# Kernel tuning notes

Measured on AMD Instinct MI355X. Metric: run time of the kernel, lower is better.

Reference implementation:

```python
import jax, jax.numpy as jnp
import numpy as np

K = 3    # spline degree
NUM = 5  # grid intervals


def _extended_grid(in_dim):
    # pykan default grid_range=[-1,1], extended by K knots of spacing h on each side
    h = 2.0 / NUM
    g = jnp.linspace(-1.0 - K * h, 1.0 + K * h, NUM + 2 * K + 1, dtype=jnp.float32)
    return jnp.tile(g[None, :], (in_dim, 1))  # (in_dim, NUM+2K+1)


def _bspline_basis(x, grid):
    # Cox-de Boor recursion, matches pykan B_batch.
    # x: (..., in_dim); grid: (in_dim, NUM+2K+1) -> (..., in_dim, NUM+K)
    xe = x[..., None]
    B = ((xe >= grid[:, :-1]) & (xe < grid[:, 1:])).astype(x.dtype)
    for d in range(1, K + 1):
        left = (xe - grid[:, :-(d + 1)]) / (grid[:, d:-1] - grid[:, :-(d + 1)])
        right = (grid[:, d + 1:] - xe) / (grid[:, d + 1:] - grid[:, 1:-d])
        B = left * B[..., :-1] + right * B[..., 1:]
    return B


def _kan_layer(x, grid, coef, scale_base, scale_sp):
    # pykan KANLayer.forward (mask == 1): y = sum_i scale_base*silu(x) + scale_sp*spline(x)
    base = jax.nn.silu(x)                              # (..., in)
    Bx = _bspline_basis(x, grid)                       # (..., in, NUM+K)
    spl = jnp.einsum('...ik,iok->...io', Bx, coef)     # (..., in, out)
    y = scale_base * base[..., None] + scale_sp * spl  # (..., in, out)
    return y.sum(axis=-2)                              # (..., out)


def setup_inputs() -> dict:
    key = jax.random.key(0)
    seq_len, in_dim, hidden_dim, out_dim = 8192, 128, 512, 128
    nb = NUM + K
    hu_in = in_dim + hidden_dim
    ks = jax.random.split(key, 5)
    return {
        "x": jax.random.normal(ks[0], (seq_len, in_dim), jnp.float32),
        "h0": jnp.zeros((hidden_dim,), jnp.float32),
        "hu_grid": _extended_grid(hu_in),
        "hu_coef": jax.random.normal(ks[1], (hu_in, hidden_dim, nb), jnp.float32) * 0.1,
        "hu_scale_base": jax.random.normal(ks[2], (hu_in, hidden_dim), jnp.float32) / np.sqrt(hu_in).astype(np.float32),
        "hu_scale_sp": jnp.ones((hu_in, hidden_dim), jnp.float32) / np.float32(np.sqrt(hu_in)),
        "out_grid": _extended_grid(hidden_dim),
        "out_coef": jax.random.normal(ks[3], (hidden_dim, out_dim, nb), jnp.float32) * 0.1,
        "out_scale_base": jax.random.normal(ks[4], (hidden_dim, out_dim), jnp.float32) / np.float32(np.sqrt(hidden_dim)),
        "out_scale_sp": jnp.ones((hidden_dim, out_dim), jnp.float32) / np.float32(np.sqrt(hidden_dim)),
    }


def reference(x, h0, hu_grid, hu_coef, hu_scale_base, hu_scale_sp,
              out_grid, out_coef, out_scale_base, out_scale_sp):
    # Sequential KAN-cell recurrence over time (torch for-loop -> lax.scan)
    def step(h, x_t):
        inp = jnp.concatenate([x_t, h])  # (in_dim + hidden_dim,)
        h_new = _kan_layer(inp, hu_grid, hu_coef, hu_scale_base, hu_scale_sp)
        return h_new, h_new

    _, hidden_states = jax.lax.scan(step, h0, x)  # (seq, hidden)
    outputs = _kan_layer(hidden_states, out_grid, out_coef, out_scale_base, out_scale_sp)
    return outputs, hidden_states
```

## Files before the change

### kernel.cpp

```cpp
#include <hip/hip_runtime.h>
#include <math.h>

#define SEQ 8192
#define IN_DIM 128
#define HID 512
#define OUT_DIM 128
#define NK 9
#define KNOTS 12

#define WS_W9HU  0
#define WS_WSEQP 589824
#define WS_XPART (WS_WSEQP + 1179648)
#define WS_HCOMM (WS_XPART + 4194304)
#define WS_TOTAL (WS_HCOMM + 4194304)

#define SENTINEL 0x7FA0DEADu

#define NWG 32
#define TPB2 512

__device__ __forceinline__ int brow(int ib) { return ib*3 + (ib >> 4); }
__device__ __forceinline__ int boff(int row) { return row*12 + ((row >> 2) << 2); }

__device__ __forceinline__ unsigned bf16rne(float f) {
    unsigned b = __float_as_uint(f);
    return (b + 0x7fffu + ((b >> 16) & 1u)) >> 16;
}
__device__ __forceinline__ float blo(unsigned p) { return __uint_as_float(p << 16); }
__device__ __forceinline__ float bhi(unsigned p) { return __uint_as_float(p & 0xffff0000u); }

__device__ __forceinline__ void load_knots(const float* gptr, float* g, float* invA) {
    #pragma unroll
    for (int j = 0; j < KNOTS; ++j) g[j] = gptr[j];
    #pragma unroll
    for (int d = 1; d <= 3; ++d) {
        #pragma unroll
        for (int j = 0; j < 11; ++j) {
            if (j + d <= 11) invA[(d-1)*11 + j] = 1.0f / (g[j+d] - g[j]);
        }
    }
}

__device__ __forceinline__ void basis9(float x, const float* g, const float* invA, float* out) {
    float B[11];
    #pragma unroll
    for (int j = 0; j < 11; ++j)
        B[j] = (x >= g[j] && x < g[j+1]) ? 1.0f : 0.0f;
    #pragma unroll
    for (int d = 1; d <= 3; ++d) {
        #pragma unroll
        for (int j = 0; j < 11; ++j) {
            if (j + d < 11) {
                float left  = (x - g[j]) * invA[(d-1)*11 + j];
                float right = (g[j+d+1] - x) * invA[(d-1)*11 + j + 1];
                B[j] = left * B[j] + right * B[j+1];
            }
        }
    }
    #pragma unroll
    for (int j = 0; j < 8; ++j) out[j] = B[j];
    out[8] = x / (1.0f + expf(-x));
}

__global__ __launch_bounds__(256) void build1_kernel(
    const float* __restrict__ hu_coef, const float* __restrict__ hu_sb, const float* __restrict__ hu_ssp,
    float* __restrict__ ws)
{
    int idx = blockIdx.x * blockDim.x + threadIdx.x;
    int stride = gridDim.x * blockDim.x;
    const int N1 = 128 * 9 * 512;
    for (int p = idx; p < N1; p += stride) {
        int o = p & 511; int k = (p >> 9) % 9; int i = p / 4608;
        float v = (k < 8) ? hu_ssp[i*HID + o] * hu_coef[(i*HID + o)*8 + k] : hu_sb[i*HID + o];
        ws[WS_W9HU + p] = v;
    }
    unsigned* WP = (unsigned*)(ws + WS_WSEQP);
    const int N2 = 32 * 512 * 72;
    for (int p = idx; p < N2; p += stride) {
        int slot = p % 72; int th = (p / 72) & 511; int blk = p / (72 * 512);
        int q = th >> 2, oq = th & 3;
        unsigned pr;
        if (slot < 64) {
            int r = slot >> 4, j = (slot >> 2) & 3, kp = slot & 3;
            int gi = IN_DIM + 4*q + r;
            int o  = blk*16 + oq*4 + j;
            float wlo = hu_ssp[gi*HID + o] * hu_coef[(gi*HID + o)*8 + 2*kp];
            float whi = hu_ssp[gi*HID + o] * hu_coef[(gi*HID + o)*8 + 2*kp + 1];
            pr = bf16rne(wlo) | (bf16rne(whi) << 16);
        } else {
            int e = slot - 64;
            int r = e >> 1, jp = e & 1;
            int gi = IN_DIM + 4*q + r;
            int o0 = blk*16 + oq*4 + 2*jp;
            int o1 = o0 + 1;
            pr = bf16rne(hu_sb[gi*HID + o0]) | (bf16rne(hu_sb[gi*HID + o1]) << 16);
        }
        WP[p] = pr;
    }
    unsigned* hc = (unsigned*)(ws + WS_HCOMM);
    for (int p = idx; p < SEQ*HID; p += stride) hc[p] = SENTINEL;
}

__global__ __launch_bounds__(256) void build2_kernel(
    const float* __restrict__ out_coef, const float* __restrict__ out_sb, const float* __restrict__ out_ssp,
    float* __restrict__ ws)
{
    int idx = blockIdx.x * blockDim.x + threadIdx.x;
    int stride = gridDim.x * blockDim.x;
    const int N = 512 * 9 * 128;
    for (int p = idx; p < N; p += stride) {
        int o = p & 127; int k = (p >> 7) % 9; int i = p / 1152;
        float v = (k < 8) ? out_ssp[i*OUT_DIM + o] * out_coef[(i*OUT_DIM + o)*8 + k] : out_sb[i*OUT_DIM + o];
        ws[WS_W9HU + p] = v;
    }
}

#define R1 4
__global__ __launch_bounds__(256) void xpart_kernel(
    const float* __restrict__ X, const float* __restrict__ hu_grid, float* __restrict__ ws)
{
    const int tid = threadIdx.x;
    const int t0 = blockIdx.x * R1;
    const float* W9 = ws + WS_W9HU;
    float* xpart = ws + WS_XPART;
    float g[KNOTS], invA[33];
    load_knots(hu_grid, g, invA);

    __shared__ float4 bas4[R1*IN_DIM*3 + (R1*IN_DIM)/16];
    #pragma unroll
    for (int rep = 0; rep < 2; ++rep) {
        int idx = tid + rep*256;
        int r = idx >> 7, i = idx & 127;
        float bv[9];
        basis9(X[(t0 + r)*IN_DIM + i], g, invA, bv);
        int rb = brow(idx);
        bas4[rb]   = make_float4(bv[0], bv[1], bv[2], bv[3]);
        bas4[rb+1] = make_float4(bv[4], bv[5], bv[6], bv[7]);
        bas4[rb+2] = make_float4(bv[8], 0.f, 0.f, 0.f);
    }
    __syncthreads();

    float acc[R1][2];
    #pragma unroll
    for (int r = 0; r < R1; ++r) { acc[r][0] = 0.f; acc[r][1] = 0.f; }

    for (int i = 0; i < IN_DIM; ++i) {
        float w1[9], w2[9];
        #pragma unroll
        for (int k = 0; k < 9; ++k) {
            w1[k] = W9[(i*NK+k)*HID + tid];
            w2[k] = W9[(i*NK+k)*HID + tid + 256];
        }
        #pragma unroll
        for (int r = 0; r < R1; ++r) {
            const float* rp = (const float*)&bas4[brow(r*IN_DIM + i)];
            float4 b0 = ((const float4*)rp)[0], b1 = ((const float4*)rp)[1];
            float b8 = rp[8];
            float s1 = w1[0]*b0.x + w1[1]*b0.y + w1[2]*b0.z + w1[3]*b0.w
                     + w1[4]*b1.x + w1[5]*b1.y + w1[6]*b1.z + w1[7]*b1.w + w1[8]*b8;
            float s2 = w2[0]*b0.x + w2[1]*b0.y + w2[2]*b0.z + w2[3]*b0.w
                     + w2[4]*b1.x + w2[5]*b1.y + w2[6]*b1.z + w2[7]*b1.w + w2[8]*b8;
            acc[r][0] += s1; acc[r][1] += s2;
        }
    }
    #pragma unroll
    for (int r = 0; r < R1; ++r) {
        xpart[(t0+r)*HID + tid]       = acc[r][0];
        xpart[(t0+r)*HID + tid + 256] = acc[r][1];
    }
}

__global__ __launch_bounds__(TPB2, 1) void seq_kernel(
    const float* __restrict__ h0, const float* __restrict__ hu_grid,
    const unsigned* __restrict__ WP,
    const float* __restrict__ xpart,
    unsigned* __restrict__ hcomm,
    float* __restrict__ hs_out)
{
    const int tid  = threadIdx.x;
    const int blk  = blockIdx.x;
    const int lane = tid & 63;
    const int wave = tid >> 6;
    const int oq   = tid & 3;
    const int q    = tid >> 2;
    const float g0 = hu_grid[0];
    const float inv_h = 1.0f / (hu_grid[1] - hu_grid[0]);

    unsigned wsp[4][4][4];
    unsigned wsl[4][2];
    {
        const uint4* Wb = (const uint4*)(WP + ((size_t)blk*512 + tid)*72);
        #pragma unroll
        for (int r = 0; r < 4; ++r) {
            #pragma unroll
            for (int j = 0; j < 4; ++j) {
                uint4 v = Wb[r*4 + j];
                wsp[r][j][0] = v.x; wsp[r][j][1] = v.y; wsp[r][j][2] = v.z; wsp[r][j][3] = v.w;
            }
        }
        uint4 s0 = Wb[16];
        uint4 s1 = Wb[17];
        wsl[0][0]=s0.x; wsl[0][1]=s0.y; wsl[1][0]=s0.z; wsl[1][1]=s0.w;
        wsl[2][0]=s1.x; wsl[2][1]=s1.y; wsl[3][0]=s1.z; wsl[3][1]=s1.w;
    }

    __shared__ float basf[6656];
    __shared__ float red[8][4][4];

    for (int t = 0; t < SEQ; ++t) {
        float xf = (tid < 16) ? xpart[(size_t)t*HID + blk*16 + tid] : 0.0f;

        float hv;
        if (t == 0) {
            hv = h0[tid];
        } else {
            const unsigned* pp = &hcomm[(size_t)(t-1)*HID + tid];
            unsigned u = __hip_atomic_load(pp, __ATOMIC_RELAXED, __HIP_MEMORY_SCOPE_AGENT);
            int sp = 0;
            while (u == SENTINEL && ++sp < (1 << 24))
                u = __hip_atomic_load(pp, __ATOMIC_RELAXED, __HIP_MEMORY_SCOPE_AGENT);
            hv = __uint_as_float(u);
        }

        {
            float* rowp = basf + boff(tid);
            float tq = (hv - g0) * inv_h;
            float cf = floorf(tq);
            float u  = tq - cf;
            int   c  = (int)cf;
            float si = hv * __builtin_amdgcn_rcpf(1.0f + __expf(-hv));
            ((float4*)rowp)[0] = make_float4(0.f, 0.f, 0.f, 0.f);
            ((float4*)rowp)[1] = make_float4(0.f, 0.f, 0.f, 0.f);
            rowp[8] = si;
            if (c >= 0 && c <= 10) {
                float um = 1.0f - u, u2 = u*u, u3 = u2*u;
                float P0 = um*um*um*(1.0f/6.0f);
                float P1 = 0.5f*u3 - u2 + (2.0f/3.0f);
                float P2 = -0.5f*u3 + 0.5f*u2 + 0.5f*u + (1.0f/6.0f);
                float P3 = u3*(1.0f/6.0f);
                int j0 = c - 3;
                if (j0     >= 0)              rowp[j0]     = P0;
                if (j0 + 1 >= 0 && j0+1 <= 7) rowp[j0 + 1] = P1;
                if (j0 + 2 >= 0 && j0+2 <= 7) rowp[j0 + 2] = P2;
                if (j0 + 3 <= 7)              rowp[j0 + 3] = P3;
            }
        }
        __syncthreads();

        float p0 = 0.f, p1 = 0.f, p2 = 0.f, p3 = 0.f;
        #pragma unroll
        for (int r = 0; r < 4; ++r) {
            const float* rp = basf + boff(4*q + r);
            float4 b0 = ((const float4*)rp)[0], b1 = ((const float4*)rp)[1];
            float b8 = rp[8];
            p0 += blo(wsp[r][0][0])*b0.x + bhi(wsp[r][0][0])*b0.y + blo(wsp[r][0][1])*b0.z + bhi(wsp[r][0][1])*b0.w
                + blo(wsp[r][0][2])*b1.x + bhi(wsp[r][0][2])*b1.y + blo(wsp[r][0][3])*b1.z + bhi(wsp[r][0][3])*b1.w
                + blo(wsl[r][0])*b8;
            p1 += blo(wsp[r][1][0])*b0.x + bhi(wsp[r][1][0])*b0.y + blo(wsp[r][1][1])*b0.z + bhi(wsp[r][1][1])*b0.w
                + blo(wsp[r][1][2])*b1.x + bhi(wsp[r][1][2])*b1.y + blo(wsp[r][1][3])*b1.z + bhi(wsp[r][1][3])*b1.w
                + bhi(wsl[r][0])*b8;
            p2 += blo(wsp[r][2][0])*b0.x + bhi(wsp[r][2][0])*b0.y + blo(wsp[r][2][1])*b0.z + bhi(wsp[r][2][1])*b0.w
                + blo(wsp[r][2][2])*b1.x + bhi(wsp[r][2][2])*b1.y + blo(wsp[r][2][3])*b1.z + bhi(wsp[r][2][3])*b1.w
                + blo(wsl[r][1])*b8;
            p3 += blo(wsp[r][3][0])*b0.x + bhi(wsp[r][3][0])*b0.y + blo(wsp[r][3][1])*b0.z + bhi(wsp[r][3][1])*b0.w
                + blo(wsp[r][3][2])*b1.x + bhi(wsp[r][3][2])*b1.y + blo(wsp[r][3][3])*b1.z + bhi(wsp[r][3][3])*b1.w
                + bhi(wsl[r][1])*b8;
        }
        #pragma unroll
        for (int d = 4; d < 64; d <<= 1) {
            p0 += __shfl_xor(p0, d, 64);
            p1 += __shfl_xor(p1, d, 64);
            p2 += __shfl_xor(p2, d, 64);
            p3 += __shfl_xor(p3, d, 64);
        }
        if (lane < 4) {
            red[wave][lane][0] = p0;
            red[wave][lane][1] = p1;
            red[wave][lane][2] = p2;
            red[wave][lane][3] = p3;
        }
        __syncthreads();
        if (tid < 16) {
            float s = xf;
            #pragma unroll
            for (int wv = 0; wv < 8; ++wv) s += red[wv][tid>>2][tid&3];
            __hip_atomic_store(&hcomm[(size_t)t*HID + blk*16 + tid], __float_as_uint(s),
                               __ATOMIC_RELAXED, __HIP_MEMORY_SCOPE_AGENT);
            hs_out[(size_t)t*HID + blk*16 + tid] = s;
        }
        __syncthreads();
    }
}

#define R3 2
__global__ __launch_bounds__(256) void outlayer_kernel(
    const float* __restrict__ out_grid, float* __restrict__ ws, float* __restrict__ d_out)
{
    const int tid = threadIdx.x;
    const int t0 = blockIdx.x * R3;
    const float* W9o = ws + WS_W9HU;
    const float* hs = d_out + (size_t)SEQ*OUT_DIM;
    float g[KNOTS], invA[33];
    load_knots(out_grid, g, invA);

    __shared__ float4 bas4[R3*HID*3 + (R3*HID)/16];
    #pragma unroll
    for (int rep = 0; rep < 4; ++rep) {
        int idx = tid + rep*256;
        int r = idx >> 9, i = idx & 511;
        float bv[9];
        basis9(hs[(size_t)(t0+r)*HID + i], g, invA, bv);
        int rb = brow(idx);
        bas4[rb]   = make_float4(bv[0], bv[1], bv[2], bv[3]);
        bas4[rb+1] = make_float4(bv[4], bv[5], bv[6], bv[7]);
        bas4[rb+2] = make_float4(bv[8], 0.f, 0.f, 0.f);
    }
    __syncthreads();

    const int oo = tid & 127;
    const int half = tid >> 7;
    float acc[R3] = {0.f, 0.f};
    for (int ii = 0; ii < 256; ++ii) {
        int i = half*256 + ii;
        float wv[9];
        #pragma unroll
        for (int k = 0; k < 9; ++k) wv[k] = W9o[(i*NK+k)*OUT_DIM + oo];
        #pragma unroll
        for (int r = 0; r < R3; ++r) {
            const float* rp = (const float*)&bas4[brow(r*HID + i)];
            float4 b0 = ((const float4*)rp)[0], b1 = ((const float4*)rp)[1];
            float b8 = rp[8];
            acc[r] += wv[0]*b0.x + wv[1]*b0.y + wv[2]*b0.z + wv[3]*b0.w
                    + wv[4]*b1.x + wv[5]*b1.y + wv[6]*b1.z + wv[7]*b1.w + wv[8]*b8;
        }
    }
    __shared__ float red[2][R3][128];
    red[half][0][oo] = acc[0];
    red[half][1][oo] = acc[1];
    __syncthreads();
    {
        int rr = tid >> 7, o2 = tid & 127;
        d_out[(size_t)(t0+rr)*OUT_DIM + o2] = red[0][rr][o2] + red[1][rr][o2];
    }
}

extern "C" void kernel_launch(void* const* d_in, const int* in_sizes, int n_in,
                              void* d_out, int out_size, void* d_ws, size_t ws_size,
                              hipStream_t stream) {
    (void)in_sizes; (void)n_in; (void)out_size; (void)ws_size;
    const float* X        = (const float*)d_in[0];
    const float* h0       = (const float*)d_in[1];
    const float* hu_grid  = (const float*)d_in[2];
    const float* hu_coef  = (const float*)d_in[3];
    const float* hu_sb    = (const float*)d_in[4];
    const float* hu_ssp   = (const float*)d_in[5];
    const float* out_grid = (const float*)d_in[6];
    const float* out_coef = (const float*)d_in[7];
    const float* out_sb   = (const float*)d_in[8];
    const float* out_ssp  = (const float*)d_in[9];
    float* out = (float*)d_out;
    float* ws  = (float*)d_ws;

    hipLaunchKernelGGL(build1_kernel, dim3(2048), dim3(256), 0, stream,
                       hu_coef, hu_sb, hu_ssp, ws);
    hipLaunchKernelGGL(xpart_kernel, dim3(SEQ/R1), dim3(256), 0, stream, X, hu_grid, ws);
    hipLaunchKernelGGL(seq_kernel, dim3(NWG), dim3(TPB2), 0, stream,
                       h0, hu_grid,
                       (const unsigned*)(ws + WS_WSEQP),
                       ws + WS_XPART,
                       (unsigned*)(ws + WS_HCOMM),
                       out + (size_t)SEQ*OUT_DIM);
    hipLaunchKernelGGL(build2_kernel, dim3(1024), dim3(256), 0, stream,
                       out_coef, out_sb, out_ssp, ws);
    hipLaunchKernelGGL(outlayer_kernel, dim3(SEQ/R3), dim3(256), 0, stream, out_grid, ws, out);
}
```

Before: 16.75 ms.

## Elect same-XCC workgroups for recurrence and poll via sc0 loads

The sequential kernel now launches many workgroups and elects 32 of them through an atomic counter, preferring workgroups on XCC 0. Others spin briefly before joining, so the chosen set likely shares one L2. If all elected blocks report the same XCC id, the hidden-state polling uses sc0 global loads, which may be served from the shared L2 rather than going to device-coherent memory, lowering per-timestep cross-block latency. Stores write the value twice, once volatile and once atomic. The change relies on XCC id hardware registers and workgroup placement behavior, and adds election overhead and a risk of correctness or deadlock if the assumptions fail.

```diff
diff --git a/kernel.cpp b/kernel.cpp
--- a/kernel.cpp
+++ b/kernel.cpp
@@ -8,16 +8,20 @@
 #define NK 9
 #define KNOTS 12
 
-#define WS_W9HU  0
-#define WS_WSEQP 589824
+#define WS_ELECT 0
+#define WS_W9HU  64
+#define WS_WSEQP (WS_W9HU + 589824)
 #define WS_XPART (WS_WSEQP + 1179648)
 #define WS_HCOMM (WS_XPART + 4194304)
 #define WS_TOTAL (WS_HCOMM + 4194304)
 
 #define SENTINEL 0x7FA0DEADu
+#define SLOT_INIT 0xFFFFFFFFu
 
 #define NWG 32
 #define TPB2 512
+#define NB_LAUNCH 512
+#define SC0_BOUND 6
 
 __device__ __forceinline__ int brow(int ib) { return ib*3 + (ib >> 4); }
 __device__ __forceinline__ int boff(int row) { return row*12 + ((row >> 2) << 2); }
@@ -29,6 +33,13 @@
 __device__ __forceinline__ float blo(unsigned p) { return __uint_as_float(p << 16); }
 __device__ __forceinline__ float bhi(unsigned p) { return __uint_as_float(p & 0xffff0000u); }
 
+__device__ __forceinline__ unsigned ld_sc0(const unsigned* p) {
+    unsigned r;
+    asm volatile("global_load_dword %0, %1, off sc0\n\ts_waitcnt vmcnt(0)"
+                 : "=v"(r) : "v"(p) : "memory");
+    return r;
+}
+
 __device__ __forceinline__ void load_knots(const float* gptr, float* g, float* invA) {
     #pragma unroll
     for (int j = 0; j < KNOTS; ++j) g[j] = gptr[j];
@@ -51,8 +62,8 @@
         #pragma unroll
         for (int j = 0; j < 11; ++j) {
             if (j + d < 11) {
-                float left  = (x - g[j]) * invA[(d-1)*11 + j];
-                float right = (g[j+d+1] - x) * invA[(d-1)*11 + j + 1];
+                float left  = (x - g[j]) / (g[j+d] - g[j]);
+                float right = (g[j+d+1] - x) / (g[j+d+1] - g[j+1]);
                 B[j] = left * B[j] + right * B[j+1];
             }
         }
@@ -68,6 +79,8 @@
 {
     int idx = blockIdx.x * blockDim.x + threadIdx.x;
     int stride = gridDim.x * blockDim.x;
+    if (idx == 0) ((unsigned*)ws)[0] = 0u;
+    else if (idx <= 32) ((unsigned*)ws)[idx] = SLOT_INIT;
     const int N1 = 128 * 9 * 512;
     for (int p = idx; p < N1; p += stride) {
         int o = p & 511; int k = (p >> 9) % 9; int i = p / 4608;
@@ -92,8 +105,7 @@
             int r = e >> 1, jp = e & 1;
             int gi = IN_DIM + 4*q + r;
             int o0 = blk*16 + oq*4 + 2*jp;
-            int o1 = o0 + 1;
-            pr = bf16rne(hu_sb[gi*HID + o0]) | (bf16rne(hu_sb[gi*HID + o1]) << 16);
+            pr = bf16rne(hu_sb[gi*HID + o0]) | (bf16rne(hu_sb[gi*HID + o0 + 1]) << 16);
         }
         WP[p] = pr;
     }
@@ -172,16 +184,51 @@
 
 __global__ __launch_bounds__(TPB2, 1) void seq_kernel(
     const float* __restrict__ h0, const float* __restrict__ hu_grid,
+    unsigned* __restrict__ el,
     const unsigned* __restrict__ WP,
     const float* __restrict__ xpart,
     unsigned* __restrict__ hcomm,
     float* __restrict__ hs_out)
 {
+    __shared__ int sh_slot, sh_mode;
     const int tid  = threadIdx.x;
-    const int blk  = blockIdx.x;
+
+    if (tid == 0) {
+        unsigned xcc;
+        asm volatile("s_getreg_b32 %0, hwreg(HW_REG_XCC_ID)" : "=s"(xcc));
+        int slot = 64;
+        if (xcc == 0u) {
+            slot = (int)__hip_atomic_fetch_add(&el[0], 1u, __ATOMIC_RELAXED, __HIP_MEMORY_SCOPE_AGENT);
+        } else {
+            unsigned long long tc0 = __builtin_amdgcn_s_memrealtime();
+            while (__builtin_amdgcn_s_memrealtime() - tc0 < 2500ull) {}
+            unsigned c = __hip_atomic_load(&el[0], __ATOMIC_RELAXED, __HIP_MEMORY_SCOPE_AGENT);
+            if (c < (unsigned)NWG)
+                slot = (int)__hip_atomic_fetch_add(&el[0], 1u, __ATOMIC_RELAXED, __HIP_MEMORY_SCOPE_AGENT);
+        }
+        int mode = 0;
+        if (slot < NWG) {
+            __hip_atomic_store(&el[1+slot], xcc, __ATOMIC_RELAXED, __HIP_MEMORY_SCOPE_AGENT);
+            int ok = 1; unsigned first = 0;
+            for (int i = 0; i < NWG; ++i) {
+                unsigned v; int sp = 0;
+                do { v = __hip_atomic_load(&el[1+i], __ATOMIC_RELAXED, __HIP_MEMORY_SCOPE_AGENT); }
+                while (v == SLOT_INIT && ++sp < (1 << 20));
+                if (v == SLOT_INIT) { ok = 0; break; }
+                if (i == 0) first = v;
+                else if (v != first) { ok = 0; break; }
+            }
+            mode = ok;
+        }
+        sh_slot = slot; sh_mode = mode;
+    }
+    __syncthreads();
+    const int blk = sh_slot;
+    const int mode = sh_mode;
+    if (blk >= NWG) return;
+
     const int lane = tid & 63;
     const int wave = tid >> 6;
-    const int oq   = tid & 3;
     const int q    = tid >> 2;
     const float g0 = hu_grid[0];
     const float inv_h = 1.0f / (hu_grid[1] - hu_grid[0]);
@@ -215,9 +262,16 @@
             hv = h0[tid];
         } else {
             const unsigned* pp = &hcomm[(size_t)(t-1)*HID + tid];
-            unsigned u = __hip_atomic_load(pp, __ATOMIC_RELAXED, __HIP_MEMORY_SCOPE_AGENT);
-            int sp = 0;
-            while (u == SENTINEL && ++sp < (1 << 24))
+            unsigned u;
+            if (mode) {
+                u = ld_sc0(pp);
+                int sp = 0;
+                while (u == SENTINEL && ++sp < SC0_BOUND) u = ld_sc0(pp);
+            } else {
+                u = __hip_atomic_load(pp, __ATOMIC_RELAXED, __HIP_MEMORY_SCOPE_AGENT);
+            }
+            int sp2 = 0;
+            while (u == SENTINEL && ++sp2 < (1 << 24))
                 u = __hip_atomic_load(pp, __ATOMIC_RELAXED, __HIP_MEMORY_SCOPE_AGENT);
             hv = __uint_as_float(u);
         }
@@ -284,8 +338,10 @@
             float s = xf;
             #pragma unroll
             for (int wv = 0; wv < 8; ++wv) s += red[wv][tid>>2][tid&3];
-            __hip_atomic_store(&hcomm[(size_t)t*HID + blk*16 + tid], __float_as_uint(s),
-                               __ATOMIC_RELAXED, __HIP_MEMORY_SCOPE_AGENT);
+            unsigned su = __float_as_uint(s);
+            unsigned* dst = &hcomm[(size_t)t*HID + blk*16 + tid];
+            *(volatile unsigned*)dst = su;
+            __hip_atomic_store(dst, su, __ATOMIC_RELAXED, __HIP_MEMORY_SCOPE_AGENT);
             hs_out[(size_t)t*HID + blk*16 + tid] = s;
         }
         __syncthreads();
@@ -364,8 +420,9 @@
     hipLaunchKernelGGL(build1_kernel, dim3(2048), dim3(256), 0, stream,
                        hu_coef, hu_sb, hu_ssp, ws);
     hipLaunchKernelGGL(xpart_kernel, dim3(SEQ/R1), dim3(256), 0, stream, X, hu_grid, ws);
-    hipLaunchKernelGGL(seq_kernel, dim3(NWG), dim3(TPB2), 0, stream,
+    hipLaunchKernelGGL(seq_kernel, dim3(NB_LAUNCH), dim3(TPB2), 0, stream,
                        h0, hu_grid,
+                       (unsigned*)ws,
                        (const unsigned*)(ws + WS_WSEQP),
                        ws + WS_XPART,
                        (unsigned*)(ws + WS_HCOMM),
```

Result: slower. 20.88 ms (+24.6%).

## Make each wave own two outputs, removing block barriers from the recurrent step

Applied to the files above, without the earlier changes.

The sequential kernel is restructured so that each wave computes two hidden outputs over all 512 hidden inputs. Each lane evaluates 8 hidden values' spline bases in registers instead of writing them to shared memory. This removes the per-step shared-memory basis table and all three __syncthreads, replacing them with a full-wave shuffle reduction. Polling of the previous hidden state now uses vectorized cache-bypassing dwordx4 loads, with a sentinel check on all 8 values and s_sleep backoff. The weight-packing layout changes to match. In exchange, each lane does more redundant basis work (8 inputs each, recomputed in every wave) and every wave polls global memory.

```diff
diff --git a/kernel.cpp b/kernel.cpp
--- a/kernel.cpp
+++ b/kernel.cpp
@@ -19,8 +19,9 @@
 #define NWG 32
 #define TPB2 512
 
+typedef unsigned uint32x4 __attribute__((ext_vector_type(4)));
+
 __device__ __forceinline__ int brow(int ib) { return ib*3 + (ib >> 4); }
-__device__ __forceinline__ int boff(int row) { return row*12 + ((row >> 2) << 2); }
 
 __device__ __forceinline__ unsigned bf16rne(float f) {
     unsigned b = __float_as_uint(f);
@@ -28,6 +29,13 @@
 }
 __device__ __forceinline__ float blo(unsigned p) { return __uint_as_float(p << 16); }
 __device__ __forceinline__ float bhi(unsigned p) { return __uint_as_float(p & 0xffff0000u); }
+
+__device__ __forceinline__ uint32x4 ld4_if(const unsigned* p) {
+    uint32x4 r;
+    asm volatile("global_load_dwordx4 %0, %1, off sc0 sc1\n\ts_waitcnt vmcnt(0)"
+                 : "=v"(r) : "v"(p) : "memory");
+    return r;
+}
 
 __device__ __forceinline__ void load_knots(const float* gptr, float* g, float* invA) {
     #pragma unroll
@@ -75,25 +83,21 @@
         ws[WS_W9HU + p] = v;
     }
     unsigned* WP = (unsigned*)(ws + WS_WSEQP);
-    const int N2 = 32 * 512 * 72;
+    const int N2 = 256 * 64 * 72;
     for (int p = idx; p < N2; p += stride) {
-        int slot = p % 72; int th = (p / 72) & 511; int blk = p / (72 * 512);
-        int q = th >> 2, oq = th & 3;
+        int slot = p % 72; int lane = (p / 72) & 63; int opair = p / (72 * 64);
         unsigned pr;
         if (slot < 64) {
-            int r = slot >> 4, j = (slot >> 2) & 3, kp = slot & 3;
-            int gi = IN_DIM + 4*q + r;
-            int o  = blk*16 + oq*4 + j;
-            float wlo = hu_ssp[gi*HID + o] * hu_coef[(gi*HID + o)*8 + 2*kp];
-            float whi = hu_ssp[gi*HID + o] * hu_coef[(gi*HID + o)*8 + 2*kp + 1];
+            int ci = slot >> 3, o = (slot >> 2) & 1, kp = slot & 3;
+            int gi = IN_DIM + ((ci < 4) ? (4*lane + ci) : (256 + 4*lane + ci - 4));
+            int oo = opair*2 + o;
+            float wlo = hu_ssp[gi*HID + oo] * hu_coef[(gi*HID + oo)*8 + 2*kp];
+            float whi = hu_ssp[gi*HID + oo] * hu_coef[(gi*HID + oo)*8 + 2*kp + 1];
             pr = bf16rne(wlo) | (bf16rne(whi) << 16);
         } else {
-            int e = slot - 64;
-            int r = e >> 1, jp = e & 1;
-            int gi = IN_DIM + 4*q + r;
-            int o0 = blk*16 + oq*4 + 2*jp;
-            int o1 = o0 + 1;
-            pr = bf16rne(hu_sb[gi*HID + o0]) | (bf16rne(hu_sb[gi*HID + o1]) << 16);
+            int ci = slot - 64;
+            int gi = IN_DIM + ((ci < 4) ? (4*lane + ci) : (256 + 4*lane + ci - 4));
+            pr = bf16rne(hu_sb[gi*HID + opair*2]) | (bf16rne(hu_sb[gi*HID + opair*2 + 1]) << 16);
         }
         WP[p] = pr;
     }
@@ -177,118 +181,118 @@
     unsigned* __restrict__ hcomm,
     float* __restrict__ hs_out)
 {
-    const int tid  = threadIdx.x;
-    const int blk  = blockIdx.x;
-    const int lane = tid & 63;
-    const int wave = tid >> 6;
-    const int oq   = tid & 3;
-    const int q    = tid >> 2;
+    const int tid   = threadIdx.x;
+    const int lane  = tid & 63;
+    const int wv    = tid >> 6;
+    const int opair = blockIdx.x * 8 + wv;
+    const int o0    = opair * 2;
     const float g0 = hu_grid[0];
     const float inv_h = 1.0f / (hu_grid[1] - hu_grid[0]);
 
-    unsigned wsp[4][4][4];
-    unsigned wsl[4][2];
+    uint32x4 Wsp[16];
+    uint32x4 Wsl0, Wsl1;
     {
-        const uint4* Wb = (const uint4*)(WP + ((size_t)blk*512 + tid)*72);
-        #pragma unroll
-        for (int r = 0; r < 4; ++r) {
+        const uint32x4* Wb4 = (const uint32x4*)(WP + ((size_t)(opair*64 + lane))*72);
+        #pragma unroll
+        for (int r = 0; r < 16; ++r) Wsp[r] = Wb4[r];
+        Wsl0 = Wb4[16]; Wsl1 = Wb4[17];
+    }
+
+    for (int t = 0; t < SEQ; ++t) {
+        float xf0 = 0.f, xf1 = 0.f;
+        if (lane == 0) {
+            float2 xf = *(const float2*)&xpart[(size_t)t*HID + o0];
+            xf0 = xf.x; xf1 = xf.y;
+        }
+
+        float hv[8];
+        if (t == 0) {
             #pragma unroll
-            for (int j = 0; j < 4; ++j) {
-                uint4 v = Wb[r*4 + j];
-                wsp[r][j][0] = v.x; wsp[r][j][1] = v.y; wsp[r][j][2] = v.z; wsp[r][j][3] = v.w;
+            for (int ci = 0; ci < 8; ++ci)
+                hv[ci] = h0[(ci < 4) ? (4*lane + ci) : (256 + 4*lane + ci - 4)];
+        } else {
+            const unsigned* base = hcomm + (size_t)(t-1)*HID;
+            const unsigned* p0 = base + 4*lane;
+            const unsigned* p1 = base + 256 + 4*lane;
+            int fails = 0;
+            for (;;) {
+                uint32x4 a = ld4_if(p0);
+                uint32x4 b = ld4_if(p1);
+                bool ok = (a.x != SENTINEL) & (a.y != SENTINEL) & (a.z != SENTINEL) & (a.w != SENTINEL)
+                        & (b.x != SENTINEL) & (b.y != SENTINEL) & (b.z != SENTINEL) & (b.w != SENTINEL);
+                if (ok) {
+                    hv[0]=__uint_as_float(a.x); hv[1]=__uint_as_float(a.y);
+                    hv[2]=__uint_as_float(a.z); hv[3]=__uint_as_float(a.w);
+                    hv[4]=__uint_as_float(b.x); hv[5]=__uint_as_float(b.y);
+                    hv[6]=__uint_as_float(b.z); hv[7]=__uint_as_float(b.w);
+                    break;
+                }
+                if (++fails > (1 << 22)) {
+                    hv[0]=__uint_as_float(a.x); hv[1]=__uint_as_float(a.y);
+                    hv[2]=__uint_as_float(a.z); hv[3]=__uint_as_float(a.w);
+                    hv[4]=__uint_as_float(b.x); hv[5]=__uint_as_float(b.y);
+                    hv[6]=__uint_as_float(b.z); hv[7]=__uint_as_float(b.w);
+                    break;
+                }
+                if (fails > 8) __builtin_amdgcn_s_sleep(1);
             }
         }
-        uint4 s0 = Wb[16];
-        uint4 s1 = Wb[17];
-        wsl[0][0]=s0.x; wsl[0][1]=s0.y; wsl[1][0]=s0.z; wsl[1][1]=s0.w;
-        wsl[2][0]=s1.x; wsl[2][1]=s1.y; wsl[3][0]=s1.z; wsl[3][1]=s1.w;
-    }
-
-    __shared__ float basf[6656];
-    __shared__ float red[8][4][4];
-
-    for (int t = 0; t < SEQ; ++t) {
-        float xf = (tid < 16) ? xpart[(size_t)t*HID + blk*16 + tid] : 0.0f;
-
-        float hv;
-        if (t == 0) {
-            hv = h0[tid];
-        } else {
-            const unsigned* pp = &hcomm[(size_t)(t-1)*HID + tid];
-            unsigned u = __hip_atomic_load(pp, __ATOMIC_RELAXED, __HIP_MEMORY_SCOPE_AGENT);
-            int sp = 0;
-            while (u == SENTINEL && ++sp < (1 << 24))
-                u = __hip_atomic_load(pp, __ATOMIC_RELAXED, __HIP_MEMORY_SCOPE_AGENT);
-            hv = __uint_as_float(u);
-        }
-
-        {
-            float* rowp = basf + boff(tid);
-            float tq = (hv - g0) * inv_h;
+
+        float a0 = 0.f, a1 = 0.f, a0b = 0.f, a1b = 0.f;
+        #pragma unroll
+        for (int ci = 0; ci < 8; ++ci) {
+            float x  = hv[ci];
+            float tq = (x - g0) * inv_h;
             float cf = floorf(tq);
-            float u  = tq - cf;
+            float uu = tq - cf;
             int   c  = (int)cf;
-            float si = hv * __builtin_amdgcn_rcpf(1.0f + __expf(-hv));
-            ((float4*)rowp)[0] = make_float4(0.f, 0.f, 0.f, 0.f);
-            ((float4*)rowp)[1] = make_float4(0.f, 0.f, 0.f, 0.f);
-            rowp[8] = si;
-            if (c >= 0 && c <= 10) {
-                float um = 1.0f - u, u2 = u*u, u3 = u2*u;
-                float P0 = um*um*um*(1.0f/6.0f);
-                float P1 = 0.5f*u3 - u2 + (2.0f/3.0f);
-                float P2 = -0.5f*u3 + 0.5f*u2 + 0.5f*u + (1.0f/6.0f);
-                float P3 = u3*(1.0f/6.0f);
-                int j0 = c - 3;
-                if (j0     >= 0)              rowp[j0]     = P0;
-                if (j0 + 1 >= 0 && j0+1 <= 7) rowp[j0 + 1] = P1;
-                if (j0 + 2 >= 0 && j0+2 <= 7) rowp[j0 + 2] = P2;
-                if (j0 + 3 <= 7)              rowp[j0 + 3] = P3;
+            float um = 1.0f - uu, u2 = uu*uu, u3 = u2*uu;
+            float P0 = um*um*um*(1.0f/6.0f);
+            float P1 = 0.5f*u3 - u2 + (2.0f/3.0f);
+            float P2 = -0.5f*u3 + 0.5f*u2 + 0.5f*uu + (1.0f/6.0f);
+            float P3 = u3*(1.0f/6.0f);
+            float b[8];
+            #pragma unroll
+            for (int k = 0; k < 8; ++k) {
+                float v = 0.f;
+                v = (c == k+3) ? P0 : v;
+                v = (c == k+2) ? P1 : v;
+                v = (c == k+1) ? P2 : v;
+                v = (c == k  ) ? P3 : v;
+                b[k] = v;
             }
-        }
-        __syncthreads();
-
-        float p0 = 0.f, p1 = 0.f, p2 = 0.f, p3 = 0.f;
-        #pragma unroll
-        for (int r = 0; r < 4; ++r) {
-            const float* rp = basf + boff(4*q + r);
-            float4 b0 = ((const float4*)rp)[0], b1 = ((const float4*)rp)[1];
-            float b8 = rp[8];
-            p0 += blo(wsp[r][0][0])*b0.x + bhi(wsp[r][0][0])*b0.y + blo(wsp[r][0][1])*b0.z + bhi(wsp[r][0][1])*b0.w
-                + blo(wsp[r][0][2])*b1.x + bhi(wsp[r][0][2])*b1.y + blo(wsp[r][0][3])*b1.z + bhi(wsp[r][0][3])*b1.w
-                + blo(wsl[r][0])*b8;
-            p1 += blo(wsp[r][1][0])*b0.x + bhi(wsp[r][1][0])*b0.y + blo(wsp[r][1][1])*b0.z + bhi(wsp[r][1][1])*b0.w
-                + blo(wsp[r][1][2])*b1.x + bhi(wsp[r][1][2])*b1.y + blo(wsp[r][1][3])*b1.z + bhi(wsp[r][1][3])*b1.w
-                + bhi(wsl[r][0])*b8;
-            p2 += blo(wsp[r][2][0])*b0.x + bhi(wsp[r][2][0])*b0.y + blo(wsp[r][2][1])*b0.z + bhi(wsp[r][2][1])*b0.w
-                + blo(wsp[r][2][2])*b1.x + bhi(wsp[r][2][2])*b1.y + blo(wsp[r][2][3])*b1.z + bhi(wsp[r][2][3])*b1.w
-                + blo(wsl[r][1])*b8;
-            p3 += blo(wsp[r][3][0])*b0.x + bhi(wsp[r][3][0])*b0.y + blo(wsp[r][3][1])*b0.z + bhi(wsp[r][3][1])*b0.w
-                + blo(wsp[r][3][2])*b1.x + bhi(wsp[r][3][2])*b1.y + blo(wsp[r][3][3])*b1.z + bhi(wsp[r][3][3])*b1.w
-                + bhi(wsl[r][1])*b8;
-        }
-        #pragma unroll
-        for (int d = 4; d < 64; d <<= 1) {
-            p0 += __shfl_xor(p0, d, 64);
-            p1 += __shfl_xor(p1, d, 64);
-            p2 += __shfl_xor(p2, d, 64);
-            p3 += __shfl_xor(p3, d, 64);
-        }
-        if (lane < 4) {
-            red[wave][lane][0] = p0;
-            red[wave][lane][1] = p1;
-            red[wave][lane][2] = p2;
-            red[wave][lane][3] = p3;
-        }
-        __syncthreads();
-        if (tid < 16) {
-            float s = xf;
-            #pragma unroll
-            for (int wv = 0; wv < 8; ++wv) s += red[wv][tid>>2][tid&3];
-            __hip_atomic_store(&hcomm[(size_t)t*HID + blk*16 + tid], __float_as_uint(s),
+            float si = x * __builtin_amdgcn_rcpf(1.0f + __expf(-x));
+            uint32x4 w0 = Wsp[ci*2 + 0];
+            uint32x4 w1 = Wsp[ci*2 + 1];
+            float s0 = blo(w0.x)*b[0] + bhi(w0.x)*b[1] + blo(w0.y)*b[2] + bhi(w0.y)*b[3]
+                     + blo(w0.z)*b[4] + bhi(w0.z)*b[5] + blo(w0.w)*b[6] + bhi(w0.w)*b[7];
+            float s1 = blo(w1.x)*b[0] + bhi(w1.x)*b[1] + blo(w1.y)*b[2] + bhi(w1.y)*b[3]
+                     + blo(w1.z)*b[4] + bhi(w1.z)*b[5] + blo(w1.w)*b[6] + bhi(w1.w)*b[7];
+            unsigned sl;
+            if      (ci == 0) sl = Wsl0.x; else if (ci == 1) sl = Wsl0.y;
+            else if (ci == 2) sl = Wsl0.z; else if (ci == 3) sl = Wsl0.w;
+            else if (ci == 4) sl = Wsl1.x; else if (ci == 5) sl = Wsl1.y;
+            else if (ci == 6) sl = Wsl1.z; else              sl = Wsl1.w;
+            s0 += blo(sl)*si;
+            s1 += bhi(sl)*si;
+            if (ci & 1) { a0b += s0; a1b += s1; } else { a0 += s0; a1 += s1; }
+        }
+        a0 += a0b; a1 += a1b;
+
+        #pragma unroll
+        for (int d = 1; d < 64; d <<= 1) {
+            a0 += __shfl_xor(a0, d, 64);
+            a1 += __shfl_xor(a1, d, 64);
+        }
+        if (lane == 0) {
+            float s0f = a0 + xf0, s1f = a1 + xf1;
+            __hip_atomic_store(&hcomm[(size_t)t*HID + o0],     __float_as_uint(s0f),
                                __ATOMIC_RELAXED, __HIP_MEMORY_SCOPE_AGENT);
-            hs_out[(size_t)t*HID + blk*16 + tid] = s;
-        }
-        __syncthreads();
+            __hip_atomic_store(&hcomm[(size_t)t*HID + o0 + 1], __float_as_uint(s1f),
+                               __ATOMIC_RELAXED, __HIP_MEMORY_SCOPE_AGENT);
+            hs_out[(size_t)t*HID + o0]     = s0f;
+            hs_out[(size_t)t*HID + o0 + 1] = s1f;
+        }
     }
 }
 
```

Measured after the change: 44.38 ms. 165% more time.

## Compute spline basis in registers and drop per-step LDS barriers in recurrence

Applied to the files above, without the earlier changes.

Each thread now loads its own 4 hidden values with one vector load that bypasses the cache, spinning until none of them holds the sentinel. It evaluates the cubic B-spline basis and SiLU in registers instead of writing a basis table to shared memory. This removes one __syncthreads per timestep, and double-buffering the reduction array removes the trailing barrier, shortening the serial critical path of the 8192-step recurrence. In exchange each hidden value's basis is recomputed redundantly by 4 threads, and the polling issues wider uncached loads.

```diff
diff --git a/kernel.cpp b/kernel.cpp
--- a/kernel.cpp
+++ b/kernel.cpp
@@ -19,8 +19,9 @@
 #define NWG 32
 #define TPB2 512
 
+typedef unsigned uint32x4 __attribute__((ext_vector_type(4)));
+
 __device__ __forceinline__ int brow(int ib) { return ib*3 + (ib >> 4); }
-__device__ __forceinline__ int boff(int row) { return row*12 + ((row >> 2) << 2); }
 
 __device__ __forceinline__ unsigned bf16rne(float f) {
     unsigned b = __float_as_uint(f);
@@ -28,6 +29,13 @@
 }
 __device__ __forceinline__ float blo(unsigned p) { return __uint_as_float(p << 16); }
 __device__ __forceinline__ float bhi(unsigned p) { return __uint_as_float(p & 0xffff0000u); }
+
+__device__ __forceinline__ uint32x4 ld4_if(const unsigned* p) {
+    uint32x4 r;
+    asm volatile("global_load_dwordx4 %0, %1, off sc0 sc1\n\ts_waitcnt vmcnt(0)"
+                 : "=v"(r) : "v"(p) : "memory");
+    return r;
+}
 
 __device__ __forceinline__ void load_knots(const float* gptr, float* g, float* invA) {
     #pragma unroll
@@ -92,8 +100,7 @@
             int r = e >> 1, jp = e & 1;
             int gi = IN_DIM + 4*q + r;
             int o0 = blk*16 + oq*4 + 2*jp;
-            int o1 = o0 + 1;
-            pr = bf16rne(hu_sb[gi*HID + o0]) | (bf16rne(hu_sb[gi*HID + o1]) << 16);
+            pr = bf16rne(hu_sb[gi*HID + o0]) | (bf16rne(hu_sb[gi*HID + o0 + 1]) << 16);
         }
         WP[p] = pr;
     }
@@ -179,9 +186,8 @@
 {
     const int tid  = threadIdx.x;
     const int blk  = blockIdx.x;
+    const int wave = tid >> 6;
     const int lane = tid & 63;
-    const int wave = tid >> 6;
-    const int oq   = tid & 3;
     const int q    = tid >> 2;
     const float g0 = hu_grid[0];
     const float inv_h = 1.0f / (hu_grid[1] - hu_grid[0]);
@@ -189,83 +195,87 @@
     unsigned wsp[4][4][4];
     unsigned wsl[4][2];
     {
-        const uint4* Wb = (const uint4*)(WP + ((size_t)blk*512 + tid)*72);
+        const uint32x4* Wb = (const uint32x4*)(WP + ((size_t)blk*512 + tid)*72);
         #pragma unroll
         for (int r = 0; r < 4; ++r) {
             #pragma unroll
             for (int j = 0; j < 4; ++j) {
-                uint4 v = Wb[r*4 + j];
+                uint32x4 v = Wb[r*4 + j];
                 wsp[r][j][0] = v.x; wsp[r][j][1] = v.y; wsp[r][j][2] = v.z; wsp[r][j][3] = v.w;
             }
         }
-        uint4 s0 = Wb[16];
-        uint4 s1 = Wb[17];
+        uint32x4 s0 = Wb[16], s1 = Wb[17];
         wsl[0][0]=s0.x; wsl[0][1]=s0.y; wsl[1][0]=s0.z; wsl[1][1]=s0.w;
         wsl[2][0]=s1.x; wsl[2][1]=s1.y; wsl[3][0]=s1.z; wsl[3][1]=s1.w;
     }
 
-    __shared__ float basf[6656];
-    __shared__ float red[8][4][4];
+    __shared__ float red[2][8][4][4];
 
     for (int t = 0; t < SEQ; ++t) {
+        const int buf = t & 1;
         float xf = (tid < 16) ? xpart[(size_t)t*HID + blk*16 + tid] : 0.0f;
 
-        float hv;
+        float hv[4];
         if (t == 0) {
-            hv = h0[tid];
+            #pragma unroll
+            for (int r = 0; r < 4; ++r) hv[r] = h0[4*q + r];
         } else {
-            const unsigned* pp = &hcomm[(size_t)(t-1)*HID + tid];
-            unsigned u = __hip_atomic_load(pp, __ATOMIC_RELAXED, __HIP_MEMORY_SCOPE_AGENT);
-            int sp = 0;
-            while (u == SENTINEL && ++sp < (1 << 24))
-                u = __hip_atomic_load(pp, __ATOMIC_RELAXED, __HIP_MEMORY_SCOPE_AGENT);
-            hv = __uint_as_float(u);
-        }
-
-        {
-            float* rowp = basf + boff(tid);
-            float tq = (hv - g0) * inv_h;
+            const unsigned* p4 = hcomm + (size_t)(t-1)*HID + 4*q;
+            int fails = 0;
+            for (;;) {
+                uint32x4 a = ld4_if(p4);
+                if ((a.x != SENTINEL) & (a.y != SENTINEL) & (a.z != SENTINEL) & (a.w != SENTINEL)) {
+                    hv[0]=__uint_as_float(a.x); hv[1]=__uint_as_float(a.y);
+                    hv[2]=__uint_as_float(a.z); hv[3]=__uint_as_float(a.w);
+                    break;
+                }
+                if (++fails > (1 << 22)) {
+                    hv[0]=__uint_as_float(a.x); hv[1]=__uint_as_float(a.y);
+                    hv[2]=__uint_as_float(a.z); hv[3]=__uint_as_float(a.w);
+                    break;
+                }
+            }
+        }
+
+        float p0 = 0.f, p1 = 0.f, p2 = 0.f, p3 = 0.f;
+        #pragma unroll
+        for (int r = 0; r < 4; ++r) {
+            float x  = hv[r];
+            float tq = (x - g0) * inv_h;
             float cf = floorf(tq);
-            float u  = tq - cf;
+            float uu = tq - cf;
             int   c  = (int)cf;
-            float si = hv * __builtin_amdgcn_rcpf(1.0f + __expf(-hv));
-            ((float4*)rowp)[0] = make_float4(0.f, 0.f, 0.f, 0.f);
-            ((float4*)rowp)[1] = make_float4(0.f, 0.f, 0.f, 0.f);
-            rowp[8] = si;
-            if (c >= 0 && c <= 10) {
-                float um = 1.0f - u, u2 = u*u, u3 = u2*u;
-                float P0 = um*um*um*(1.0f/6.0f);
-                float P1 = 0.5f*u3 - u2 + (2.0f/3.0f);
-                float P2 = -0.5f*u3 + 0.5f*u2 + 0.5f*u + (1.0f/6.0f);
-                float P3 = u3*(1.0f/6.0f);
-                int j0 = c - 3;
-                if (j0     >= 0)              rowp[j0]     = P0;
-                if (j0 + 1 >= 0 && j0+1 <= 7) rowp[j0 + 1] = P1;
-                if (j0 + 2 >= 0 && j0+2 <= 7) rowp[j0 + 2] = P2;
-                if (j0 + 3 <= 7)              rowp[j0 + 3] = P3;
+            float um = 1.0f - uu, u2 = uu*uu, u3 = u2*uu;
+            float P0 = um*um*um*(1.0f/6.0f);
+            float P1 = 0.5f*u3 - u2 + (2.0f/3.0f);
+            float P2 = -0.5f*u3 + 0.5f*u2 + 0.5f*uu + (1.0f/6.0f);
+            float P3 = u3*(1.0f/6.0f);
+            float b[9];
+            #pragma unroll
+            for (int k = 0; k < 8; ++k) {
+                float v = 0.f;
+                v = (c == k+3) ? P0 : v;
+                v = (c == k+2) ? P1 : v;
+                v = (c == k+1) ? P2 : v;
+                v = (c == k  ) ? P3 : v;
+                b[k] = v;
             }
-        }
-        __syncthreads();
-
-        float p0 = 0.f, p1 = 0.f, p2 = 0.f, p3 = 0.f;
-        #pragma unroll
-        for (int r = 0; r < 4; ++r) {
-            const float* rp = basf + boff(4*q + r);
-            float4 b0 = ((const float4*)rp)[0], b1 = ((const float4*)rp)[1];
-            float b8 = rp[8];
-            p0 += blo(wsp[r][0][0])*b0.x + bhi(wsp[r][0][0])*b0.y + blo(wsp[r][0][1])*b0.z + bhi(wsp[r][0][1])*b0.w
-                + blo(wsp[r][0][2])*b1.x + bhi(wsp[r][0][2])*b1.y + blo(wsp[r][0][3])*b1.z + bhi(wsp[r][0][3])*b1.w
-                + blo(wsl[r][0])*b8;
-            p1 += blo(wsp[r][1][0])*b0.x + bhi(wsp[r][1][0])*b0.y + blo(wsp[r][1][1])*b0.z + bhi(wsp[r][1][1])*b0.w
-                + blo(wsp[r][1][2])*b1.x + bhi(wsp[r][1][2])*b1.y + blo(wsp[r][1][3])*b1.z + bhi(wsp[r][1][3])*b1.w
-                + bhi(wsl[r][0])*b8;
-            p2 += blo(wsp[r][2][0])*b0.x + bhi(wsp[r][2][0])*b0.y + blo(wsp[r][2][1])*b0.z + bhi(wsp[r][2][1])*b0.w
-                + blo(wsp[r][2][2])*b1.x + bhi(wsp[r][2][2])*b1.y + blo(wsp[r][2][3])*b1.z + bhi(wsp[r][2][3])*b1.w
-                + blo(wsl[r][1])*b8;
-            p3 += blo(wsp[r][3][0])*b0.x + bhi(wsp[r][3][0])*b0.y + blo(wsp[r][3][1])*b0.z + bhi(wsp[r][3][1])*b0.w
-                + blo(wsp[r][3][2])*b1.x + bhi(wsp[r][3][2])*b1.y + blo(wsp[r][3][3])*b1.z + bhi(wsp[r][3][3])*b1.w
-                + bhi(wsl[r][1])*b8;
-        }
+            b[8] = x * __builtin_amdgcn_rcpf(1.0f + __expf(-x));
+
+            p0 += blo(wsp[r][0][0])*b[0] + bhi(wsp[r][0][0])*b[1] + blo(wsp[r][0][1])*b[2] + bhi(wsp[r][0][1])*b[3]
+                + blo(wsp[r][0][2])*b[4] + bhi(wsp[r][0][2])*b[5] + blo(wsp[r][0][3])*b[6] + bhi(wsp[r][0][3])*b[7]
+                + blo(wsl[r][0])*b[8];
+            p1 += blo(wsp[r][1][0])*b[0] + bhi(wsp[r][1][0])*b[1] + blo(wsp[r][1][1])*b[2] + bhi(wsp[r][1][1])*b[3]
+                + blo(wsp[r][1][2])*b[4] + bhi(wsp[r][1][2])*b[5] + blo(wsp[r][1][3])*b[6] + bhi(wsp[r][1][3])*b[7]
+                + bhi(wsl[r][0])*b[8];
+            p2 += blo(wsp[r][2][0])*b[0] + bhi(wsp[r][2][0])*b[1] + blo(wsp[r][2][1])*b[2] + bhi(wsp[r][2][1])*b[3]
+                + blo(wsp[r][2][2])*b[4] + bhi(wsp[r][2][2])*b[5] + blo(wsp[r][2][3])*b[6] + bhi(wsp[r][2][3])*b[7]
+                + blo(wsl[r][1])*b[8];
+            p3 += blo(wsp[r][3][0])*b[0] + bhi(wsp[r][3][0])*b[1] + blo(wsp[r][3][1])*b[2] + bhi(wsp[r][3][1])*b[3]
+                + blo(wsp[r][3][2])*b[4] + bhi(wsp[r][3][2])*b[5] + blo(wsp[r][3][3])*b[6] + bhi(wsp[r][3][3])*b[7]
+                + bhi(wsl[r][1])*b[8];
+        }
+
         #pragma unroll
         for (int d = 4; d < 64; d <<= 1) {
             p0 += __shfl_xor(p0, d, 64);
@@ -274,21 +284,20 @@
             p3 += __shfl_xor(p3, d, 64);
         }
         if (lane < 4) {
-            red[wave][lane][0] = p0;
-            red[wave][lane][1] = p1;
-            red[wave][lane][2] = p2;
-            red[wave][lane][3] = p3;
+            red[buf][wave][lane][0] = p0;
+            red[buf][wave][lane][1] = p1;
+            red[buf][wave][lane][2] = p2;
+            red[buf][wave][lane][3] = p3;
         }
         __syncthreads();
         if (tid < 16) {
             float s = xf;
             #pragma unroll
-            for (int wv = 0; wv < 8; ++wv) s += red[wv][tid>>2][tid&3];
+            for (int wv = 0; wv < 8; ++wv) s += red[buf][wv][tid>>2][tid&3];
             __hip_atomic_store(&hcomm[(size_t)t*HID + blk*16 + tid], __float_as_uint(s),
                                __ATOMIC_RELAXED, __HIP_MEMORY_SCOPE_AGENT);
             hs_out[(size_t)t*HID + blk*16 + tid] = s;
         }
-        __syncthreads();
     }
 }
 
```

New measurement: 20.44 ms. 22.0% more time.
